# Performance work log

Hardware: AMD Instinct MI355X
Metric: run time of the kernel (lower is better)

## Reference

```python
import jax, jax.numpy as jnp
import numpy as np

CHANNELS = 512
NUM_HEADS = 8
NUM_GROUPS = 32
EPS = 1e-5


def setup_inputs() -> dict:
    key = jax.random.key(0)
    ks = jax.random.split(key, 6)
    c = CHANNELS
    x = jax.random.normal(ks[0], (8, c, 32, 32), dtype=jnp.float32)
    norm_w = jnp.ones((c,), jnp.float32)
    norm_b = jnp.zeros((c,), jnp.float32)
    # 1x1 conv1d weights stored as [out, in]
    qkv_w = jax.random.normal(ks[1], (3 * c, c), jnp.float32) * (1.0 / np.sqrt(c))
    qkv_b = jax.random.normal(ks[2], (3 * c,), jnp.float32) * 0.02
    # proj_out is zero-initialized in the original; use small random values so the
    # residual branch is exercised numerically (init values are not part of the math).
    proj_w = jax.random.normal(ks[3], (c, c), jnp.float32) * 0.02
    proj_b = jax.random.normal(ks[4], (c,), jnp.float32) * 0.02
    return {"x": x, "norm_w": norm_w, "norm_b": norm_b,
            "qkv_w": qkv_w, "qkv_b": qkv_b, "proj_w": proj_w, "proj_b": proj_b}


def _group_norm(x, w, b):
    # x: [B, C, L]; normalize per (batch, group) over (C/G, L) in float32
    B, C, L = x.shape
    xg = x.astype(jnp.float32).reshape(B, NUM_GROUPS, (C // NUM_GROUPS) * L)
    mean = xg.mean(axis=-1, keepdims=True)
    var = xg.var(axis=-1, keepdims=True)
    xn = ((xg - mean) * jax.lax.rsqrt(var + EPS)).reshape(B, C, L)
    return (xn * w[None, :, None] + b[None, :, None]).astype(x.dtype)


def _attention_legacy(qkv, n_heads):
    # qkv: [B, 3*C, L]  (QKVAttentionLegacy: split heads after reshape)
    B, width, L = qkv.shape
    ch = width // (3 * n_heads)
    q, k, v = jnp.split(qkv.reshape(B * n_heads, 3 * ch, L), 3, axis=1)
    scale = 1.0 / np.sqrt(np.sqrt(ch))
    w = jnp.einsum('bct,bcs->bts', q * scale, k * scale)  # [B*H, L, L]
    w = jax.nn.softmax(w.astype(jnp.float32), axis=-1).astype(qkv.dtype)
    a = jnp.einsum('bts,bcs->bct', w, v)  # [B*H, ch, L]
    return a.reshape(B, n_heads * ch, L)


def reference(x, norm_w, norm_b, qkv_w, qkv_b, proj_w, proj_b):
    b, c = x.shape[0], x.shape[1]
    spatial = x.shape[2:]
    x_ = x.reshape(b, c, -1)  # [B, C, L]
    xn = _group_norm(x_, norm_w, norm_b)
    qkv = jnp.einsum('oc,bcl->bol', qkv_w, xn) + qkv_b[None, :, None]
    h = _attention_legacy(qkv, NUM_HEADS)
    h = jnp.einsum('oc,bcl->bol', proj_w, h) + proj_b[None, :, None]
    return (x_ + h).reshape(b, c, *spatial)
```

## Files before the change

kernel.cpp:

```cpp
#include <hip/hip_runtime.h>
#include <hip/hip_bf16.h>
#include <stdint.h>


#define NB 8
#define NC 512
#define NL 1024
#define NHD 8
#define ND 64

typedef __attribute__((ext_vector_type(4))) float f32x4;
typedef __attribute__((ext_vector_type(8))) short bf16x8;
typedef __attribute__((ext_vector_type(4))) short bf16x4;
typedef __attribute__((ext_vector_type(4))) unsigned short u16x4;
typedef __attribute__((ext_vector_type(8))) unsigned short u16x8;

#define MFMA16(a, b, c) __builtin_amdgcn_mfma_f32_16x16x32_bf16((a), (b), (c), 0, 0, 0)

static __device__ __forceinline__ f32x4 mfma_k16(bf16x4 a, bf16x4 b, f32x4 c) {
#if __has_builtin(__builtin_amdgcn_mfma_f32_16x16x16bf16_1k)
  return __builtin_amdgcn_mfma_f32_16x16x16bf16_1k(a, b, c, 0, 0, 0);
#else
  asm("v_mfma_f32_16x16x16_bf16 %0, %1, %2, %0" : "+v"(c) : "v"(a), "v"(b));
  return c;
#endif
}

#if __has_builtin(__builtin_amdgcn_exp2f)
#define EXP2F __builtin_amdgcn_exp2f
#else
#define EXP2F exp2f
#endif

static __device__ __forceinline__ unsigned short f2bf(float f) {
  union { float f; uint32_t u; } v; v.f = f;
  uint32_t r = v.u + 0x7fffu + ((v.u >> 16) & 1u);
  return (unsigned short)(r >> 16);
}

static __device__ __forceinline__ short f2bf_h(float f) {
  __hip_bfloat16 h = __float2bfloat16(f);
  return *reinterpret_cast<short*>(&h);
}

static __device__ __forceinline__ void gl_lds16(const unsigned short* g, unsigned short* l) {
  __builtin_amdgcn_global_load_lds(
      (const __attribute__((address_space(1))) void*)g,
      (__attribute__((address_space(3))) void*)l, 16, 0, 0);
}

__global__ __launch_bounds__(256) void k_pre(const float* __restrict__ x,
                                             const float* __restrict__ nw,
                                             const float* __restrict__ nb,
                                             const float* __restrict__ qkvw,
                                             const float* __restrict__ pw,
                                             unsigned short* __restrict__ xnt,
                                             unsigned short* __restrict__ qwb,
                                             unsigned short* __restrict__ pwb) {
  if (blockIdx.x >= 256) {
    int i = (blockIdx.x - 256) * 256 + threadIdx.x;
    const int NQ4 = (3 * NC * NC) / 4;
    if (i < NQ4) {
      f32x4 v = ((const f32x4*)qkvw)[i];
      u16x4 o; o.x = f2bf(v.x); o.y = f2bf(v.y); o.z = f2bf(v.z); o.w = f2bf(v.w);
      ((u16x4*)qwb)[i] = o;
    } else {
      int j = i - NQ4;
      f32x4 v = ((const f32x4*)pw)[j];
      u16x4 o; o.x = f2bf(v.x); o.y = f2bf(v.y); o.z = f2bf(v.z); o.w = f2bf(v.w);
      ((u16x4*)pwb)[j] = o;
    }
    return;
  }
  const int b = blockIdx.x >> 5, g = blockIdx.x & 31;
  const float* base = x + ((size_t)b * NC + g * 16) * NL;
  const int t = threadIdx.x;
  f32x4 vals[16];
  float s = 0.f, ss = 0.f;
#pragma unroll
  for (int r = 0; r < 16; ++r) {
    f32x4 v = ((const f32x4*)base)[t + 256 * r];
    vals[r] = v;
    s += v.x + v.y + v.z + v.w;
    ss += v.x * v.x + v.y * v.y + v.z * v.z + v.w * v.w;
  }
#pragma unroll
  for (int m = 1; m < 64; m <<= 1) { s += __shfl_xor(s, m, 64); ss += __shfl_xor(ss, m, 64); }
  __shared__ float red[8];
  const int w = t >> 6;
  if ((t & 63) == 0) { red[w] = s; red[4 + w] = ss; }
  __syncthreads();
  s  = red[0] + red[1] + red[2] + red[3];
  ss = red[4] + red[5] + red[6] + red[7];
  const float mean = s * (1.f / 16384.f);
  const float var  = ss * (1.f / 16384.f) - mean * mean;
  const float inv  = rsqrtf(var + 1e-5f);
  u16x8 ov[4][2];
#pragma unroll
  for (int r = 0; r < 16; ++r) {
    float wcv = nw[g * 16 + r] * inv;
    float bcv = nb[g * 16 + r] - mean * wcv;
    f32x4 v = vals[r];
    ov[0][r >> 3][r & 7] = f2bf(v.x * wcv + bcv);
    ov[1][r >> 3][r & 7] = f2bf(v.y * wcv + bcv);
    ov[2][r >> 3][r & 7] = f2bf(v.z * wcv + bcv);
    ov[3][r >> 3][r & 7] = f2bf(v.w * wcv + bcv);
  }
#pragma unroll
  for (int j = 0; j < 4; ++j) {
    size_t off = ((size_t)b * NL + 4 * t + j) * NC + g * 16;
    *(u16x8*)(xnt + off)     = ov[j][0];
    *(u16x8*)(xnt + off + 8) = ov[j][1];
  }
}

__global__ __launch_bounds__(256) void k_qkv(const unsigned short* __restrict__ xnt,
                                             const unsigned short* __restrict__ qwb,
                                             const float* __restrict__ qkvb,
                                             unsigned short* __restrict__ qt,
                                             unsigned short* __restrict__ kt,
                                             unsigned short* __restrict__ vt) {
  __shared__ __align__(16) unsigned short As[2][128 * 64];
  __shared__ __align__(16) unsigned short Bs[2][128 * 64];
  const int m0 = blockIdx.x * 128;
  const int n0 = blockIdx.y * 128;
  const int b = blockIdx.z;
  const int tid = threadIdx.x, lane = tid & 63, w = tid >> 6;
  const int wr = w >> 1, wc = w & 1;
  const int lo = lane & 15, g = lane >> 4;

  int soff[4];
#pragma unroll
  for (int r = 0; r < 4; ++r) {
    int c = (r * 4 + w) * 64 + lane;
    int row = c >> 3, lc = (c & 7) ^ (row & 7);
    soff[r] = row * NC + lc * 8;
  }
  const unsigned short* Ap = xnt + (size_t)b * NL * NC + (size_t)m0 * NC;
  const unsigned short* Bp = qwb + (size_t)n0 * NC;

  f32x4 acc[4][4];
#pragma unroll
  for (int mi = 0; mi < 4; ++mi)
#pragma unroll
    for (int ni = 0; ni < 4; ++ni) acc[mi][ni] = (f32x4){0.f, 0.f, 0.f, 0.f};

#pragma unroll
  for (int r = 0; r < 4; ++r) {
    gl_lds16(Ap + soff[r], &As[0][(r * 4 + w) * 512]);
    gl_lds16(Bp + soff[r], &Bs[0][(r * 4 + w) * 512]);
  }
  Ap += 64; Bp += 64;

#define QKV_KS(BUF, KS)                                                       \
  {                                                                           \
    bf16x8 af[4], bfr[4];                                                     \
    _Pragma("unroll")                                                         \
    for (int mi = 0; mi < 4; ++mi) {                                          \
      int row = wr * 64 + mi * 16 + lo;                                       \
      int ph = (g + (KS) * 4) ^ (row & 7);                                    \
      af[mi] = *(const bf16x8*)&As[BUF][row * 64 + ph * 8];                   \
    }                                                                         \
    _Pragma("unroll")                                                         \
    for (int ni = 0; ni < 4; ++ni) {                                          \
      int row = wc * 64 + ni * 16 + lo;                                       \
      int ph = (g + (KS) * 4) ^ (row & 7);                                    \
      bfr[ni] = *(const bf16x8*)&Bs[BUF][row * 64 + ph * 8];                  \
    }                                                                         \
    _Pragma("unroll")                                                         \
    for (int mi = 0; mi < 4; ++mi)                                            \
      _Pragma("unroll")                                                       \
      for (int ni = 0; ni < 4; ++ni)                                          \
        acc[mi][ni] = MFMA16(af[mi], bfr[ni], acc[mi][ni]);                   \
  }

#define QKV_STEP(BUF, LAST)                                                   \
  {                                                                           \
    __syncthreads();                                                          \
    if (!(LAST)) {                                                            \
      _Pragma("unroll")                                                       \
      for (int r = 0; r < 4; ++r)                                             \
        gl_lds16(Ap + soff[r], &As[(BUF) ^ 1][(r * 4 + w) * 512]);            \
    }                                                                         \
    QKV_KS(BUF, 0);                                                           \
    if (!(LAST)) {                                                            \
      _Pragma("unroll")                                                       \
      for (int r = 0; r < 4; ++r)                                             \
        gl_lds16(Bp + soff[r], &Bs[(BUF) ^ 1][(r * 4 + w) * 512]);            \
      Ap += 64; Bp += 64;                                                     \
    }                                                                         \
    QKV_KS(BUF, 1);                                                           \
  }

  for (int it = 0; it < 8; it += 2) {
    QKV_STEP(0, false);
    QKV_STEP(1, it == 6);
  }
#undef QKV_STEP
#undef QKV_KS

#pragma unroll
  for (int ni = 0; ni < 4; ++ni) {
    int o = n0 + wc * 64 + ni * 16 + lo;
    int head = o / 192, rem = o - head * 192;
    int type = rem >> 6, ch = rem & 63;
    float bias = qkvb[o];
#pragma unroll
    for (int mi = 0; mi < 4; ++mi) {
      int l0 = m0 + wr * 64 + mi * 16 + (g << 2);
      if (type == 2) {
        u16x4 pk;
#pragma unroll
        for (int i = 0; i < 4; ++i) pk[i] = f2bf(acc[mi][ni][i] + bias);
        *(u16x4*)&vt[(((size_t)(b * NHD + head) * 256 + (l0 >> 2)) * ND + ch) * 4] = pk;
      } else {
        const float sc = (type == 0)
            ? (0.35355339059327373f * 1.4426950408889634f)
            : 0.35355339059327373f;
        unsigned short* dst =
            (type == 0 ? qt : kt) + ((size_t)(b * NHD + head) * NL + l0) * ND + ch;
#pragma unroll
        for (int i = 0; i < 4; ++i)
          dst[i * ND] = f2bf((acc[mi][ni][i] + bias) * sc);
      }
    }
  }
}

__global__ __launch_bounds__(256) void k_attn(const unsigned short* __restrict__ qt,
                                              const unsigned short* __restrict__ kt,
                                              const unsigned short* __restrict__ vt,
                                              unsigned short* __restrict__ abuf) {
  __shared__ __align__(16) unsigned short Ks[2][128 * 64];
  __shared__ __align__(16) unsigned short Vs[2][128 * 64];
  const int bid = blockIdx.x;
  const int bh = (bid & 7) * 8 + (bid >> 6);
  const int tb = (bid >> 3) & 7;
  const int tid = threadIdx.x, lane = tid & 63, w = tid >> 6;
  const int lo = lane & 15, g = lane >> 4;
  const int t0 = tb * 128 + w * 32;
  const unsigned short* qb = qt + (size_t)bh * NL * ND;

  int koff[4], voff[4];
#pragma unroll
  for (int r = 0; r < 4; ++r) {
    int c = (r * 4 + w) * 64 + lane;
    int row = c >> 3, lc = (c & 7) ^ (row & 7);
    koff[r] = row * ND + lc * 8;
    voff[r] = c * 8;
  }
  const int e0 = lo * 64 + ((g ^ (lo & 7)) * 8);
  const int e1 = lo * 64 + (((4 + g) ^ (lo & 7)) * 8);
  const int vbase = g * 256 + lo * 4;

  const unsigned short* kst = kt + (size_t)bh * NL * ND;
  const unsigned short* vst = vt + (size_t)bh * NL * ND;

  bf16x8 qf[2][2];
#pragma unroll
  for (int h = 0; h < 2; ++h)
#pragma unroll
    for (int ks = 0; ks < 2; ++ks)
      qf[h][ks] = *(const bf16x8*)&qb[(size_t)(t0 + h * 16 + lo) * ND + ks * 32 + g * 8];

  bf16x4 vones;
#pragma unroll
  for (int j = 0; j < 4; ++j) vones[j] = (short)0x3F80;

  f32x4 pv[2][4];
#pragma unroll
  for (int h = 0; h < 2; ++h)
#pragma unroll
    for (int ci = 0; ci < 4; ++ci) pv[h][ci] = (f32x4){0.f, 0.f, 0.f, 0.f};
  f32x4 lacc[2];
  lacc[0] = (f32x4){0.f, 0.f, 0.f, 0.f};
  lacc[1] = (f32x4){0.f, 0.f, 0.f, 0.f};

#pragma unroll
  for (int r = 0; r < 4; ++r) {
    gl_lds16(kst + koff[r], &Ks[0][(r * 4 + w) * 512]);
    gl_lds16(vst + voff[r], &Vs[0][(r * 4 + w) * 512]);
  }
  kst += 8192; vst += 8192;

#define ATTN_HALF(BUF, HH)                                                    \
  {                                                                           \
    f32x4 sacc[2][4];                                                         \
    _Pragma("unroll")                                                         \
    for (int h = 0; h < 2; ++h)                                               \
      _Pragma("unroll")                                                       \
      for (int sblk = 0; sblk < 4; ++sblk)                                    \
        sacc[h][sblk] = (f32x4){0.f, 0.f, 0.f, 0.f};                          \
    __builtin_amdgcn_s_setprio(1);                                            \
    _Pragma("unroll")                                                         \
    for (int sblk = 0; sblk < 4; ++sblk) {                                    \
      bf16x8 kf = *(const bf16x8*)&Ks[BUF][(HH) * 4096 + sblk * 1024 + e0];   \
      sacc[0][sblk] = MFMA16(kf, qf[0][0], sacc[0][sblk]);                    \
      sacc[1][sblk] = MFMA16(kf, qf[1][0], sacc[1][sblk]);                    \
    }                                                                         \
    _Pragma("unroll")                                                         \
    for (int sblk = 0; sblk < 4; ++sblk) {                                    \
      bf16x8 kf = *(const bf16x8*)&Ks[BUF][(HH) * 4096 + sblk * 1024 + e1];   \
      sacc[0][sblk] = MFMA16(kf, qf[0][1], sacc[0][sblk]);                    \
      sacc[1][sblk] = MFMA16(kf, qf[1][1], sacc[1][sblk]);                    \
    }                                                                         \
    __builtin_amdgcn_s_setprio(0);                                            \
    _Pragma("unroll")                                                         \
    for (int sblk = 0; sblk < 4; ++sblk) {                                    \
      float a0 = EXP2F(sacc[0][sblk][0]);                                     \
      float a1 = EXP2F(sacc[0][sblk][1]);                                     \
      float a2 = EXP2F(sacc[0][sblk][2]);                                     \
      float a3 = EXP2F(sacc[0][sblk][3]);                                     \
      bf16x4 pf0;                                                             \
      pf0[0] = f2bf_h(a0); pf0[1] = f2bf_h(a1);                               \
      pf0[2] = f2bf_h(a2); pf0[3] = f2bf_h(a3);                               \
      float b0 = EXP2F(sacc[1][sblk][0]);                                     \
      float b1 = EXP2F(sacc[1][sblk][1]);                                     \
      float b2 = EXP2F(sacc[1][sblk][2]);                                     \
      float b3 = EXP2F(sacc[1][sblk][3]);                                     \
      bf16x4 pf1;                                                             \
      pf1[0] = f2bf_h(b0); pf1[1] = f2bf_h(b1);                               \
      pf1[2] = f2bf_h(b2); pf1[3] = f2bf_h(b3);                               \
      __builtin_amdgcn_s_setprio(1);                                          \
      lacc[0] = mfma_k16(pf0, vones, lacc[0]);                                \
      lacc[1] = mfma_k16(pf1, vones, lacc[1]);                                \
      _Pragma("unroll")                                                       \
      for (int ci = 0; ci < 4; ++ci) {                                        \
        bf16x4 vf = *(const bf16x4*)                                          \
            &Vs[BUF][(HH) * 4096 + sblk * 1024 + ci * 64 + vbase];            \
        pv[0][ci] = mfma_k16(pf0, vf, pv[0][ci]);                             \
        pv[1][ci] = mfma_k16(pf1, vf, pv[1][ci]);                             \
      }                                                                       \
      __builtin_amdgcn_s_setprio(0);                                          \
    }                                                                         \
  }

#define ATTN_TILE(BUF, LAST)                                                  \
  {                                                                           \
    __syncthreads();                                                          \
    if (!(LAST)) {                                                            \
      _Pragma("unroll")                                                       \
      for (int r = 0; r < 4; ++r)                                             \
        gl_lds16(kst + koff[r], &Ks[(BUF) ^ 1][(r * 4 + w) * 512]);           \
    }                                                                         \
    ATTN_HALF(BUF, 0);                                                        \
    if (!(LAST)) {                                                            \
      _Pragma("unroll")                                                       \
      for (int r = 0; r < 4; ++r)                                             \
        gl_lds16(vst + voff[r], &Vs[(BUF) ^ 1][(r * 4 + w) * 512]);           \
      kst += 8192; vst += 8192;                                               \
    }                                                                         \
    ATTN_HALF(BUF, 1);                                                        \
  }

  for (int it = 0; it < 8; it += 2) {
    ATTN_TILE(0, false);
    ATTN_TILE(1, it == 6);
  }
#undef ATTN_TILE
#undef ATTN_HALF

#pragma unroll
  for (int h = 0; h < 2; ++h) {
    float li[4];
#pragma unroll
    for (int i = 0; i < 4; ++i) li[i] = 1.0f / lacc[h][i];
#pragma unroll
    for (int ci = 0; ci < 4; ++ci)
#pragma unroll
      for (int i = 0; i < 4; ++i) {
        int tl = t0 + h * 16 + g * 4 + i;
        abuf[((size_t)bh * NL + tl) * ND + ci * 16 + lo] = f2bf_h(pv[h][ci][i] * li[i]);
      }
  }
}

__global__ __launch_bounds__(256) void k_proj(const unsigned short* __restrict__ abuf,
                                              const unsigned short* __restrict__ pwb,
                                              const float* __restrict__ pb,
                                              const float* __restrict__ x,
                                              float* __restrict__ out) {
  __shared__ __align__(16) unsigned short As[2][128 * 64];
  __shared__ __align__(16) unsigned short Bs[2][128 * 64];
  const int m0 = blockIdx.x * 128;
  const int n0 = blockIdx.y * 128;
  const int b = blockIdx.z;
  const int tid = threadIdx.x, lane = tid & 63, w = tid >> 6;
  const int wr = w >> 1, wc = w & 1;
  const int lo = lane & 15, g = lane >> 4;

  int aoff[4], boff[4];
#pragma unroll
  for (int r = 0; r < 4; ++r) {
    int c = (r * 4 + w) * 64 + lane;
    int row = c >> 3, lc = (c & 7) ^ (row & 7);
    aoff[r] = row * NC + lc * 8;
    boff[r] = row * ND + lc * 8;
  }
  const unsigned short* Ap = pwb + (size_t)m0 * NC;
  const unsigned short* Bp = abuf + ((size_t)(b * NHD) * NL + n0) * ND;

  f32x4 acc[4][4];
#pragma unroll
  for (int mi = 0; mi < 4; ++mi)
#pragma unroll
    for (int ni = 0; ni < 4; ++ni) acc[mi][ni] = (f32x4){0.f, 0.f, 0.f, 0.f};

#pragma unroll
  for (int r = 0; r < 4; ++r) {
    gl_lds16(Ap + aoff[r], &As[0][(r * 4 + w) * 512]);
    gl_lds16(Bp + boff[r], &Bs[0][(r * 4 + w) * 512]);
  }
  Ap += 64; Bp += (size_t)NL * ND;

#define PROJ_KS(BUF, KS)                                                      \
  {                                                                           \
    bf16x8 af[4], bfr[4];                                                     \
    _Pragma("unroll")                                                         \
    for (int mi = 0; mi < 4; ++mi) {                                          \
      int row = wr * 64 + mi * 16 + lo;                                       \
      int ph = (g + (KS) * 4) ^ (row & 7);                                    \
      af[mi] = *(const bf16x8*)&As[BUF][row * 64 + ph * 8];                   \
    }                                                                         \
    _Pragma("unroll")                                                         \
    for (int ni = 0; ni < 4; ++ni) {                                          \
      int row = wc * 64 + ni * 16 + lo;                                       \
      int ph = (g + (KS) * 4) ^ (row & 7);                                    \
      bfr[ni] = *(const bf16x8*)&Bs[BUF][row * 64 + ph * 8];                  \
    }                                                                         \
    _Pragma("unroll")                                                         \
    for (int mi = 0; mi < 4; ++mi)                                            \
      _Pragma("unroll")                                                       \
      for (int ni = 0; ni < 4; ++ni)                                          \
        acc[mi][ni] = MFMA16(af[mi], bfr[ni], acc[mi][ni]);                   \
  }

#define PROJ_STEP(BUF, LAST)                                                  \
  {                                                                           \
    __syncthreads();                                                          \
    if (!(LAST)) {                                                            \
      _Pragma("unroll")                                                       \
      for (int r = 0; r < 4; ++r)                                             \
        gl_lds16(Ap + aoff[r], &As[(BUF) ^ 1][(r * 4 + w) * 512]);            \
    }                                                                         \
    PROJ_KS(BUF, 0);                                                          \
    if (!(LAST)) {                                                            \
      _Pragma("unroll")                                                       \
      for (int r = 0; r < 4; ++r)                                             \
        gl_lds16(Bp + boff[r], &Bs[(BUF) ^ 1][(r * 4 + w) * 512]);            \
      Ap += 64; Bp += (size_t)NL * ND;                                        \
    }                                                                         \
    PROJ_KS(BUF, 1);                                                          \
  }

  for (int it = 0; it < 8; it += 2) {
    PROJ_STEP(0, false);
    PROJ_STEP(1, it == 6);
  }
#undef PROJ_STEP
#undef PROJ_KS

#pragma unroll
  for (int mi = 0; mi < 4; ++mi)
#pragma unroll
    for (int i = 0; i < 4; ++i) {
      int o = m0 + wr * 64 + mi * 16 + g * 4 + i;
      float pbv = pb[o];
#pragma unroll
      for (int ni = 0; ni < 4; ++ni) {
        int l = n0 + wc * 64 + ni * 16 + lo;
        size_t idx = ((size_t)b * NC + o) * NL + l;
        out[idx] = x[idx] + acc[mi][ni][i] + pbv;
      }
    }
}

extern "C" void kernel_launch(void* const* d_in, const int* in_sizes, int n_in,
                              void* d_out, int out_size, void* d_ws, size_t ws_size,
                              hipStream_t stream) {
  const float* x    = (const float*)d_in[0];
  const float* nw   = (const float*)d_in[1];
  const float* nb   = (const float*)d_in[2];
  const float* qkvw = (const float*)d_in[3];
  const float* qkvb = (const float*)d_in[4];
  const float* pw   = (const float*)d_in[5];
  const float* pb   = (const float*)d_in[6];
  float* out = (float*)d_out;

  char* ws = (char*)d_ws;
  unsigned short* xnt  = (unsigned short*)(ws);
  unsigned short* abuf = (unsigned short*)(ws);
  unsigned short* qwb  = (unsigned short*)(ws + 8388608);
  unsigned short* pwb  = (unsigned short*)(ws + 9961472);
  unsigned short* qt   = (unsigned short*)(ws + 10485760);
  unsigned short* kt   = (unsigned short*)(ws + 18874368);
  unsigned short* vt   = (unsigned short*)(ws + 27262976);

  k_pre<<<1280, 256, 0, stream>>>(x, nw, nb, qkvw, pw, xnt, qwb, pwb);
  k_qkv<<<dim3(8, 12, 8), 256, 0, stream>>>(xnt, qwb, qkvb, qt, kt, vt);
  k_attn<<<512, 256, 0, stream>>>(qt, kt, vt, abuf);
  k_proj<<<dim3(4, 8, 8), 256, 0, stream>>>(abuf, pwb, pb, x, out);
}
```

Measured before the change: 77.78 us.

## Switch attention K/V staging to triple-buffered 64-row tiles with vmcnt waits

The attention kernel now stages K and V in 64-key tiles across three LDS buffers instead of two 128-key buffers. Loads are issued two tiles ahead, and each step waits with an explicit s_waitcnt vmcnt plus s_barrier rather than a full __syncthreads. The goal is deeper prefetch that hides global-to-LDS latency, with LDS use dropping from 64KB to 48KB, which may help occupancy. The loop is fully unrolled over 16 iterations, which risks code bloat, and it relies on the vmcnt counts being exact for correctness.

```diff
diff --git a/kernel.cpp b/kernel.cpp
--- a/kernel.cpp
+++ b/kernel.cpp
@@ -231,8 +231,8 @@
                                               const unsigned short* __restrict__ kt,
                                               const unsigned short* __restrict__ vt,
                                               unsigned short* __restrict__ abuf) {
-  __shared__ __align__(16) unsigned short Ks[2][128 * 64];
-  __shared__ __align__(16) unsigned short Vs[2][128 * 64];
+  __shared__ __align__(16) unsigned short Ks[3][64 * 64];
+  __shared__ __align__(16) unsigned short Vs[3][64 * 64];
   const int bid = blockIdx.x;
   const int bh = (bid & 7) * 8 + (bid >> 6);
   const int tb = (bid >> 3) & 7;
@@ -241,9 +241,9 @@
   const int t0 = tb * 128 + w * 32;
   const unsigned short* qb = qt + (size_t)bh * NL * ND;
 
-  int koff[4], voff[4];
-#pragma unroll
-  for (int r = 0; r < 4; ++r) {
+  int koff[2], voff[2];
+#pragma unroll
+  for (int r = 0; r < 2; ++r) {
     int c = (r * 4 + w) * 64 + lane;
     int row = c >> 3, lc = (c & 7) ^ (row & 7);
     koff[r] = row * ND + lc * 8;
@@ -277,13 +277,15 @@
   lacc[1] = (f32x4){0.f, 0.f, 0.f, 0.f};
 
 #pragma unroll
-  for (int r = 0; r < 4; ++r) {
-    gl_lds16(kst + koff[r], &Ks[0][(r * 4 + w) * 512]);
-    gl_lds16(vst + voff[r], &Vs[0][(r * 4 + w) * 512]);
-  }
-  kst += 8192; vst += 8192;
-
-#define ATTN_HALF(BUF, HH)                                                    \
+  for (int p = 0; p < 2; ++p) {
+    gl_lds16(kst + koff[0], &Ks[p][w * 512]);
+    gl_lds16(kst + koff[1], &Ks[p][(4 + w) * 512]);
+    gl_lds16(vst + voff[0], &Vs[p][w * 512]);
+    gl_lds16(vst + voff[1], &Vs[p][(4 + w) * 512]);
+    kst += 4096; vst += 4096;
+  }
+
+#define ATTN_BODY(BUF)                                                        \
   {                                                                           \
     f32x4 sacc[2][4];                                                         \
     _Pragma("unroll")                                                         \
@@ -294,13 +296,13 @@
     __builtin_amdgcn_s_setprio(1);                                            \
     _Pragma("unroll")                                                         \
     for (int sblk = 0; sblk < 4; ++sblk) {                                    \
-      bf16x8 kf = *(const bf16x8*)&Ks[BUF][(HH) * 4096 + sblk * 1024 + e0];   \
+      bf16x8 kf = *(const bf16x8*)&Ks[BUF][sblk * 1024 + e0];                 \
       sacc[0][sblk] = MFMA16(kf, qf[0][0], sacc[0][sblk]);                    \
       sacc[1][sblk] = MFMA16(kf, qf[1][0], sacc[1][sblk]);                    \
     }                                                                         \
     _Pragma("unroll")                                                         \
     for (int sblk = 0; sblk < 4; ++sblk) {                                    \
-      bf16x8 kf = *(const bf16x8*)&Ks[BUF][(HH) * 4096 + sblk * 1024 + e1];   \
+      bf16x8 kf = *(const bf16x8*)&Ks[BUF][sblk * 1024 + e1];                 \
       sacc[0][sblk] = MFMA16(kf, qf[0][1], sacc[0][sblk]);                    \
       sacc[1][sblk] = MFMA16(kf, qf[1][1], sacc[1][sblk]);                    \
     }                                                                         \
@@ -326,8 +328,7 @@
       lacc[1] = mfma_k16(pf1, vones, lacc[1]);                                \
       _Pragma("unroll")                                                       \
       for (int ci = 0; ci < 4; ++ci) {                                        \
-        bf16x4 vf = *(const bf16x4*)                                          \
-            &Vs[BUF][(HH) * 4096 + sblk * 1024 + ci * 64 + vbase];            \
+        bf16x4 vf = *(const bf16x4*)&Vs[BUF][sblk * 1024 + ci * 64 + vbase];  \
         pv[0][ci] = mfma_k16(pf0, vf, pv[0][ci]);                             \
         pv[1][ci] = mfma_k16(pf1, vf, pv[1][ci]);                             \
       }                                                                       \
@@ -335,30 +336,27 @@
     }                                                                         \
   }
 
-#define ATTN_TILE(BUF, LAST)                                                  \
-  {                                                                           \
-    __syncthreads();                                                          \
-    if (!(LAST)) {                                                            \
-      _Pragma("unroll")                                                       \
-      for (int r = 0; r < 4; ++r)                                             \
-        gl_lds16(kst + koff[r], &Ks[(BUF) ^ 1][(r * 4 + w) * 512]);           \
-    }                                                                         \
-    ATTN_HALF(BUF, 0);                                                        \
-    if (!(LAST)) {                                                            \
-      _Pragma("unroll")                                                       \
-      for (int r = 0; r < 4; ++r)                                             \
-        gl_lds16(vst + voff[r], &Vs[(BUF) ^ 1][(r * 4 + w) * 512]);           \
-      kst += 8192; vst += 8192;                                               \
-    }                                                                         \
-    ATTN_HALF(BUF, 1);                                                        \
-  }
-
-  for (int it = 0; it < 8; it += 2) {
-    ATTN_TILE(0, false);
-    ATTN_TILE(1, it == 6);
-  }
-#undef ATTN_TILE
-#undef ATTN_HALF
+#pragma unroll
+  for (int it = 0; it < 16; ++it) {
+    const int buf = it % 3;
+    if (it < 15) {
+      asm volatile("s_waitcnt vmcnt(4)" ::: "memory");
+    } else {
+      asm volatile("s_waitcnt vmcnt(0)" ::: "memory");
+    }
+    __builtin_amdgcn_s_barrier();
+    __builtin_amdgcn_sched_barrier(0);
+    if (it < 14) {
+      const int nb = (it + 2) % 3;
+      gl_lds16(kst + koff[0], &Ks[nb][w * 512]);
+      gl_lds16(kst + koff[1], &Ks[nb][(4 + w) * 512]);
+      gl_lds16(vst + voff[0], &Vs[nb][w * 512]);
+      gl_lds16(vst + voff[1], &Vs[nb][(4 + w) * 512]);
+      kst += 4096; vst += 4096;
+    }
+    ATTN_BODY(buf);
+  }
+#undef ATTN_BODY
 
 #pragma unroll
   for (int h = 0; h < 2; ++h) {
```

Measured after the change: 78.46 us. Within noise of the previous version (+0.9%).
